# Kernel optimization log

Hardware: AMD Instinct MI355X
Metric: run time of the kernel (lower is better)

## Reference

```python
import jax, jax.numpy as jnp
import numpy as np

B, P, C = 256, 256, 512
EPS = 1e-6

def setup_inputs() -> dict:
    key = jax.random.key(0)
    ks = jax.random.split(key, 9)
    s_p = 1.0 / np.sqrt(P)
    s_c = 1.0 / np.sqrt(C)
    return {
        "x": jax.random.normal(ks[0], (B, P, C), dtype=jnp.float32),
        "ln_g": jnp.ones((C,), jnp.float32),
        "ln_b": jnp.zeros((C,), jnp.float32),
        # token-mixing MLP (P -> P -> P)
        "w1a": jax.random.normal(ks[1], (P, P), jnp.float32) * s_p,
        "b1a": jnp.zeros((P,), jnp.float32),
        "w1b": jax.random.normal(ks[2], (P, P), jnp.float32) * s_p,
        "b1b": jnp.zeros((P,), jnp.float32),
        # channel-mixing MLP (C -> C -> C)
        "w2a": jax.random.normal(ks[3], (C, C), jnp.float32) * s_c,
        "b2a": jnp.zeros((C,), jnp.float32),
        "w2b": jax.random.normal(ks[4], (C, C), jnp.float32) * s_c,
        "b2b": jnp.zeros((C,), jnp.float32),
    }

def _layernorm(v, g, b):
    mu = jnp.mean(v, axis=-1, keepdims=True)
    var = jnp.mean(jnp.square(v - mu), axis=-1, keepdims=True)
    return (v - mu) * jax.lax.rsqrt(var + EPS) * g + b

def reference(x, ln_g, ln_b, w1a, b1a, w1b, b1b, w2a, b2a, w2b, b2b):
    # token mixing: normalize, transpose to [B, C, P], MLP over P, transpose back
    h = _layernorm(x, ln_g, ln_b)                       # [B, P, C]
    ht = jnp.swapaxes(h, 1, 2)                          # [B, C, P]
    t = jax.nn.gelu(ht @ w1a + b1a, approximate=False) @ w1b + b1b
    x = jnp.swapaxes(t, 1, 2) + x                       # residual with original input
    # channel mixing: note residual adds to the NORMALIZED x (as in source)
    h = _layernorm(x, ln_g, ln_b)                       # [B, P, C]
    t2 = jax.nn.gelu(h @ w2a + b2a, approximate=False) @ w2b + b2b
    return h + t2
```

## Files before the change

### kernel.cpp

```cpp
#include <hip/hip_runtime.h>
#include <hip/hip_bf16.h>
#include <math.h>

typedef __bf16 bf16x8 __attribute__((ext_vector_type(8)));
typedef float f32x4 __attribute__((ext_vector_type(4)));
typedef unsigned short u16x8 __attribute__((ext_vector_type(8)));

#define DEV __device__ __forceinline__

DEV unsigned short f2bf(float f){ __hip_bfloat16 h=__float2bfloat16(f); unsigned short u; __builtin_memcpy(&u,&h,2); return u; }
DEV float bf2f(unsigned short u){ __hip_bfloat16 h; __builtin_memcpy(&h,&u,2); return __bfloat162float(h); }

DEV float gelu_f(float v){
  float u = v*(0.7978845608f + 0.0356774081f*v*v);
  float e = __expf(2.0f*u);
  float t = 1.0f - 2.0f*__builtin_amdgcn_rcpf(e + 1.0f);
  return 0.5f*v*(1.0f + t);
}

DEV void gl2lds16(const void* g, void* l){
  __builtin_amdgcn_global_load_lds((const __attribute__((address_space(1))) void*)g,
                                   (__attribute__((address_space(3))) void*)l, 16, 0, 0);
}

__global__ __launch_bounds__(256) void k_wt(const float* __restrict__ W,
                                            unsigned short* __restrict__ WT,
                                            int K, int N){
  int i = blockIdx.x*256 + threadIdx.x;
  if (i >= K*N) return;
  int k = i % K, n = i / K;
  WT[i] = f2bf(W[(size_t)k*N + n]);
}

__global__ __launch_bounds__(256) void k_ln1x(const float* __restrict__ x,
                                              const float* __restrict__ g,
                                              const float* __restrict__ be,
                                              unsigned short* __restrict__ ht,
                                              unsigned short* __restrict__ xb){
  __shared__ unsigned short tile[32][512];
  int blk = blockIdx.x;
  int b = blk >> 3, p0 = (blk & 7) << 5;
  int tid = threadIdx.x, w = tid >> 6, l = tid & 63;
  float4 gv0 = *(const float4*)(g  + l*8);
  float4 gv1 = *(const float4*)(g  + l*8 + 4);
  float4 bv0 = *(const float4*)(be + l*8);
  float4 bv1 = *(const float4*)(be + l*8 + 4);
  const float* xbase = x + (((size_t)b << 8) + p0) * 512;
  for (int i = 0; i < 8; ++i) {
    int pl = (i << 2) + w;
    const float* row = xbase + (size_t)pl*512 + l*8;
    float4 v0 = *(const float4*)row;
    float4 v1 = *(const float4*)(row + 4);
    u16x8 rc;
    rc[0]=f2bf(v0.x); rc[1]=f2bf(v0.y); rc[2]=f2bf(v0.z); rc[3]=f2bf(v0.w);
    rc[4]=f2bf(v1.x); rc[5]=f2bf(v1.y); rc[6]=f2bf(v1.z); rc[7]=f2bf(v1.w);
    *(u16x8*)(xb + (((size_t)b << 8) + p0 + pl)*512 + l*8) = rc;
    float s  = v0.x+v0.y+v0.z+v0.w + v1.x+v1.y+v1.z+v1.w;
    float s2 = v0.x*v0.x+v0.y*v0.y+v0.z*v0.z+v0.w*v0.w
             + v1.x*v1.x+v1.y*v1.y+v1.z*v1.z+v1.w*v1.w;
    #pragma unroll
    for (int off = 32; off; off >>= 1){ s += __shfl_xor(s, off); s2 += __shfl_xor(s2, off); }
    float mu = s * (1.0f/512.0f);
    float rs = rsqrtf(s2*(1.0f/512.0f) - mu*mu + 1e-6f);
    u16x8 o;
    o[0]=f2bf((v0.x-mu)*rs*gv0.x+bv0.x);
    o[1]=f2bf((v0.y-mu)*rs*gv0.y+bv0.y);
    o[2]=f2bf((v0.z-mu)*rs*gv0.z+bv0.z);
    o[3]=f2bf((v0.w-mu)*rs*gv0.w+bv0.w);
    o[4]=f2bf((v1.x-mu)*rs*gv1.x+bv1.x);
    o[5]=f2bf((v1.y-mu)*rs*gv1.y+bv1.y);
    o[6]=f2bf((v1.z-mu)*rs*gv1.z+bv1.z);
    o[7]=f2bf((v1.w-mu)*rs*gv1.w+bv1.w);
    *(u16x8*)(&tile[pl][l*8]) = o;
  }
  __syncthreads();
  unsigned short* hb = ht + ((size_t)b << 17);
  #pragma unroll
  for (int it = 0; it < 8; ++it) {
    int c = (it << 6) + (tid >> 2);
    int pch = (tid & 3) << 3;
    u16x8 o;
    #pragma unroll
    for (int j = 0; j < 8; ++j) o[j] = tile[pch + j][c];
    *(u16x8*)(hb + (size_t)c*256 + p0 + pch) = o;
  }
}

__global__ __launch_bounds__(256) void k_tl2(const unsigned short* __restrict__ t,
                                             const unsigned short* __restrict__ xb,
                                             const float* __restrict__ g,
                                             const float* __restrict__ be,
                                             unsigned short* __restrict__ h2){
  __shared__ unsigned short th[32][520];
  int blk = blockIdx.x;
  int b = blk >> 3, p0 = (blk & 7) << 5;
  int tid = threadIdx.x, w = tid >> 6, l = tid & 63;
  const unsigned short* tb = t + ((size_t)b << 17) + p0;
  #pragma unroll
  for (int it = 0; it < 8; ++it){
    int fc = (it << 8) + tid;
    int c = fc >> 2, pch = (fc & 3) << 3;
    u16x8 tv = *(const u16x8*)(tb + (size_t)c*256 + pch);
    #pragma unroll
    for (int j = 0; j < 8; ++j) th[pch + j][c] = tv[j];
  }
  __syncthreads();
  float4 gv0 = *(const float4*)(g  + l*8);
  float4 gv1 = *(const float4*)(g  + l*8 + 4);
  float4 bv0 = *(const float4*)(be + l*8);
  float4 bv1 = *(const float4*)(be + l*8 + 4);
  #pragma unroll
  for (int it = 0; it < 8; ++it){
    int pl = (it << 2) + w;
    u16x8 tvv = *(const u16x8*)(&th[pl][l*8]);
    size_t rowo = (((size_t)b << 8) + p0 + pl)*512 + l*8;
    u16x8 xvv = *(const u16x8*)(xb + rowo);
    float v[8];
    #pragma unroll
    for (int j = 0; j < 8; ++j) v[j] = bf2f(tvv[j]) + bf2f(xvv[j]);
    float s = 0.f, s2 = 0.f;
    #pragma unroll
    for (int j = 0; j < 8; ++j){ s += v[j]; s2 += v[j]*v[j]; }
    #pragma unroll
    for (int off = 32; off; off >>= 1){ s += __shfl_xor(s, off); s2 += __shfl_xor(s2, off); }
    float mu = s * (1.0f/512.0f);
    float rs = rsqrtf(s2*(1.0f/512.0f) - mu*mu + 1e-6f);
    u16x8 o;
    o[0]=f2bf((v[0]-mu)*rs*gv0.x+bv0.x);
    o[1]=f2bf((v[1]-mu)*rs*gv0.y+bv0.y);
    o[2]=f2bf((v[2]-mu)*rs*gv0.z+bv0.z);
    o[3]=f2bf((v[3]-mu)*rs*gv0.w+bv0.w);
    o[4]=f2bf((v[4]-mu)*rs*gv1.x+bv1.x);
    o[5]=f2bf((v[5]-mu)*rs*gv1.y+bv1.y);
    o[6]=f2bf((v[6]-mu)*rs*gv1.z+bv1.z);
    o[7]=f2bf((v[7]-mu)*rs*gv1.w+bv1.w);
    *(u16x8*)(h2 + rowo) = o;
  }
}

template<int N, int KT, int MODE>
__global__ __launch_bounds__(256, 2) void k_gemm(
    const unsigned short* __restrict__ A,
    const unsigned short* __restrict__ BT,
    const float* __restrict__ bias,
    unsigned short* __restrict__ outb,
    float* __restrict__ outf,
    const unsigned short* __restrict__ res)
{
  constexpr int K = KT*64;
  constexpr int nTn = N/128;
  constexpr int EPITCH = 176;
  constexpr int EREG   = 64*EPITCH;
  __shared__ char lds[4*EREG];
  char* lsA = lds;
  char* lsB = lds + 16384;

  int nwg = gridDim.x, bid = blockIdx.x;
  int wgid = ((nwg & 7) == 0) ? ((bid & 7)*(nwg >> 3) + (bid >> 3)) : bid;
  int tm = wgid / nTn, tn = wgid % nTn;
  size_t m0 = (size_t)tm * 128;
  int n0 = tn * 128;

  const int tid = threadIdx.x;
  const int w = tid >> 6, l = tid & 63;
  const int wm = w >> 1, wn = w & 1;
  const int la = l & 15, lg = l >> 4;

  f32x4 acc[4][4];
  #pragma unroll
  for (int i = 0; i < 4; ++i)
    #pragma unroll
    for (int j = 0; j < 4; ++j) acc[i][j] = (f32x4){0.f,0.f,0.f,0.f};

  for (int kt = 0; kt < KT; ++kt){
    int kb = kt << 6;
    #pragma unroll
    for (int i = 0; i < 4; ++i){
      int q = (i << 8) + tid;
      int row = q >> 3, sc = q & 7;
      int cc = sc ^ (row & 7);
      gl2lds16(A  + (m0 + row)*K + kb + (cc << 3), lsA + q*16);
      gl2lds16(BT + (size_t)(n0 + row)*K + kb + (cc << 3), lsB + q*16);
    }
    __syncthreads();
    #pragma unroll
    for (int ks = 0; ks < 2; ++ks){
      int c = (ks << 2) + lg;
      bf16x8 af[4], bfr[4];
      #pragma unroll
      for (int mi = 0; mi < 4; ++mi){
        int rr = (wm << 6) + (mi << 4) + la;
        af[mi] = *(const bf16x8*)(lsA + ((rr << 3) + (c ^ (rr & 7)))*16);
      }
      #pragma unroll
      for (int ni = 0; ni < 4; ++ni){
        int rn = (wn << 6) + (ni << 4) + la;
        bfr[ni] = *(const bf16x8*)(lsB + ((rn << 3) + (c ^ (rn & 7)))*16);
      }
      #pragma unroll
      for (int mi = 0; mi < 4; ++mi)
        #pragma unroll
        for (int ni = 0; ni < 4; ++ni)
          acc[mi][ni] = __builtin_amdgcn_mfma_f32_16x16x32_bf16(af[mi], bfr[ni], acc[mi][ni], 0, 0, 0);
    }
    __syncthreads();
  }

  char* ep = lds + w*EREG;
  #pragma unroll
  for (int ni = 0; ni < 4; ++ni){
    int colw = (ni << 4) + la;
    float bv = bias[n0 + (wn << 6) + colw];
    #pragma unroll
    for (int mi = 0; mi < 4; ++mi){
      #pragma unroll
      for (int rg = 0; rg < 4; ++rg){
        float v = acc[mi][ni][rg] + bv;
        if (MODE == 0) v = gelu_f(v);
        int r = (mi << 4) + (lg << 2) + rg;
        *(unsigned short*)(ep + r*EPITCH + colw*2) = f2bf(v);
      }
    }
  }
  __syncthreads();

  #pragma unroll
  for (int i = 0; i < 8; ++i){
    int q = (i << 8) + tid;
    int r = q >> 4, ck = q & 15;
    int wreg = ((r >> 6) << 1) | (ck >> 3);
    u16x8 val = *(const u16x8*)(lds + wreg*EREG + (r & 63)*EPITCH + (ck & 7)*16);
    size_t go = (m0 + r)*N + n0 + (ck << 3);
    if (MODE != 2){
      *(u16x8*)(outb + go) = val;
    } else {
      u16x8 rv = *(const u16x8*)(res + go);
      float4 o0, o1;
      o0.x = bf2f(val[0]) + bf2f(rv[0]);
      o0.y = bf2f(val[1]) + bf2f(rv[1]);
      o0.z = bf2f(val[2]) + bf2f(rv[2]);
      o0.w = bf2f(val[3]) + bf2f(rv[3]);
      o1.x = bf2f(val[4]) + bf2f(rv[4]);
      o1.y = bf2f(val[5]) + bf2f(rv[5]);
      o1.z = bf2f(val[6]) + bf2f(rv[6]);
      o1.w = bf2f(val[7]) + bf2f(rv[7]);
      *(float4*)(outf + go)     = o0;
      *(float4*)(outf + go + 4) = o1;
    }
  }
}

extern "C" void kernel_launch(void* const* d_in, const int* in_sizes, int n_in,
                              void* d_out, int out_size, void* d_ws, size_t ws_size,
                              hipStream_t stream) {
  const float* x   = (const float*)d_in[0];
  const float* lng = (const float*)d_in[1];
  const float* lnb = (const float*)d_in[2];
  const float* w1a = (const float*)d_in[3];
  const float* b1a = (const float*)d_in[4];
  const float* w1b = (const float*)d_in[5];
  const float* b1b = (const float*)d_in[6];
  const float* w2a = (const float*)d_in[7];
  const float* b2a = (const float*)d_in[8];
  const float* w2b = (const float*)d_in[9];
  const float* b2b = (const float*)d_in[10];
  float* out = (float*)d_out;
  char* ws = (char*)d_ws;
  unsigned short* bufA = (unsigned short*)ws;
  unsigned short* bufB = (unsigned short*)(ws + (size_t)(64u << 20));
  unsigned short* wt1a = (unsigned short*)(ws + (size_t)(128u << 20));
  unsigned short* wt1b = wt1a + 256*256;
  unsigned short* wt2a = wt1b + 256*256;
  unsigned short* wt2b = wt2a + 512*512;
  unsigned short* xb   = (unsigned short*)d_out;

  k_wt<<<256,  256, 0, stream>>>(w1a, wt1a, 256, 256);
  k_wt<<<256,  256, 0, stream>>>(w1b, wt1b, 256, 256);
  k_wt<<<1024, 256, 0, stream>>>(w2a, wt2a, 512, 512);
  k_wt<<<1024, 256, 0, stream>>>(w2b, wt2b, 512, 512);

  k_ln1x<<<2048, 256, 0, stream>>>(x, lng, lnb, bufA, xb);
  k_gemm<256, 4, 0><<<2048, 256, 0, stream>>>(bufA, wt1a, b1a, bufB, nullptr, nullptr);
  k_gemm<256, 4, 1><<<2048, 256, 0, stream>>>(bufB, wt1b, b1b, bufA, nullptr, nullptr);

  k_tl2<<<2048, 256, 0, stream>>>(bufA, xb, lng, lnb, bufB);

  k_gemm<512, 8, 0><<<2048, 256, 0, stream>>>(bufB, wt2a, b2a, bufA, nullptr, nullptr);
  k_gemm<512, 8, 2><<<2048, 256, 0, stream>>>(bufA, wt2b, b2b, nullptr, out, bufB);
}
```

Baseline: 293.2 us.

## Compute second token GEMM transposed to drop transpose in LN2 kernel

Replaces the second token-mixing GEMM with a transposed GEMM (W1b^T times activations) that writes its output directly in [B,P,C] layout. The LN2 kernel then becomes a simple row-wise, grid-strided pass with no LDS transpose. The change also merges the four weight-transpose launches into one kernel, and adds an XOR swizzle to the LN1 transpose tile to reduce LDS bank conflicts. The transposed GEMM reads the weights as the A operand and the activations as B, which may change the L2 reuse pattern.

```diff
diff --git a/kernel.cpp b/kernel.cpp
--- a/kernel.cpp
+++ b/kernel.cpp
@@ -23,13 +23,28 @@
                                    (__attribute__((address_space(3))) void*)l, 16, 0, 0);
 }
 
-__global__ __launch_bounds__(256) void k_wt(const float* __restrict__ W,
-                                            unsigned short* __restrict__ WT,
-                                            int K, int N){
+__global__ __launch_bounds__(256) void k_wt4(const float* __restrict__ w1a,
+                                             const float* __restrict__ w1b,
+                                             const float* __restrict__ w2a,
+                                             const float* __restrict__ w2b,
+                                             unsigned short* __restrict__ o1a,
+                                             unsigned short* __restrict__ o1b,
+                                             unsigned short* __restrict__ o2a,
+                                             unsigned short* __restrict__ o2b){
   int i = blockIdx.x*256 + threadIdx.x;
-  if (i >= K*N) return;
-  int k = i % K, n = i / K;
-  WT[i] = f2bf(W[(size_t)k*N + n]);
+  const float* W; unsigned short* O; int KN, j;
+  if (i < 131072){
+    if (i < 65536){ W = w1a; O = o1a; j = i; }
+    else          { W = w1b; O = o1b; j = i - 65536; }
+    KN = 256;
+  } else {
+    int i2 = i - 131072;
+    if (i2 < 262144){ W = w2a; O = o2a; j = i2; }
+    else            { W = w2b; O = o2b; j = i2 - 262144; }
+    KN = 512;
+  }
+  int k = j % KN, n = j / KN;
+  O[j] = f2bf(W[(size_t)k*KN + n]);
 }
 
 __global__ __launch_bounds__(256) void k_ln1x(const float* __restrict__ x,
@@ -46,6 +61,7 @@
   float4 bv0 = *(const float4*)(be + l*8);
   float4 bv1 = *(const float4*)(be + l*8 + 4);
   const float* xbase = x + (((size_t)b << 8) + p0) * 512;
+  #pragma unroll
   for (int i = 0; i < 8; ++i) {
     int pl = (i << 2) + w;
     const float* row = xbase + (size_t)pl*512 + l*8;
@@ -71,58 +87,45 @@
     o[5]=f2bf((v1.y-mu)*rs*gv1.y+bv1.y);
     o[6]=f2bf((v1.z-mu)*rs*gv1.z+bv1.z);
     o[7]=f2bf((v1.w-mu)*rs*gv1.w+bv1.w);
-    *(u16x8*)(&tile[pl][l*8]) = o;
+    *(u16x8*)(&tile[pl][(l ^ ((pl >> 3) << 1)) << 3]) = o;
   }
   __syncthreads();
   unsigned short* hb = ht + ((size_t)b << 17);
   #pragma unroll
   for (int it = 0; it < 8; ++it) {
     int c = (it << 6) + (tid >> 2);
-    int pch = (tid & 3) << 3;
+    int q = tid & 3, pch = q << 3;
+    int cs = c ^ (q << 4);
     u16x8 o;
     #pragma unroll
-    for (int j = 0; j < 8; ++j) o[j] = tile[pch + j][c];
+    for (int j = 0; j < 8; ++j) o[j] = tile[pch + j][cs];
     *(u16x8*)(hb + (size_t)c*256 + p0 + pch) = o;
   }
 }
 
-__global__ __launch_bounds__(256) void k_tl2(const unsigned short* __restrict__ t,
-                                             const unsigned short* __restrict__ xb,
-                                             const float* __restrict__ g,
-                                             const float* __restrict__ be,
-                                             unsigned short* __restrict__ h2){
-  __shared__ unsigned short th[32][520];
-  int blk = blockIdx.x;
-  int b = blk >> 3, p0 = (blk & 7) << 5;
+__global__ __launch_bounds__(256) void k_tl2s(const unsigned short* __restrict__ t,
+                                              const unsigned short* __restrict__ xb,
+                                              const float* __restrict__ g,
+                                              const float* __restrict__ be,
+                                              unsigned short* __restrict__ h2){
   int tid = threadIdx.x, w = tid >> 6, l = tid & 63;
-  const unsigned short* tb = t + ((size_t)b << 17) + p0;
-  #pragma unroll
-  for (int it = 0; it < 8; ++it){
-    int fc = (it << 8) + tid;
-    int c = fc >> 2, pch = (fc & 3) << 3;
-    u16x8 tv = *(const u16x8*)(tb + (size_t)c*256 + pch);
-    #pragma unroll
-    for (int j = 0; j < 8; ++j) th[pch + j][c] = tv[j];
-  }
-  __syncthreads();
   float4 gv0 = *(const float4*)(g  + l*8);
   float4 gv1 = *(const float4*)(g  + l*8 + 4);
   float4 bv0 = *(const float4*)(be + l*8);
   float4 bv1 = *(const float4*)(be + l*8 + 4);
-  #pragma unroll
-  for (int it = 0; it < 8; ++it){
-    int pl = (it << 2) + w;
-    u16x8 tvv = *(const u16x8*)(&th[pl][l*8]);
-    size_t rowo = (((size_t)b << 8) + p0 + pl)*512 + l*8;
-    u16x8 xvv = *(const u16x8*)(xb + rowo);
+  int wid = blockIdx.x*4 + w;
+  for (int r = wid; r < 65536; r += gridDim.x*4){
+    size_t off = (size_t)r*512 + l*8;
+    u16x8 tv = *(const u16x8*)(t + off);
+    u16x8 xv = *(const u16x8*)(xb + off);
     float v[8];
     #pragma unroll
-    for (int j = 0; j < 8; ++j) v[j] = bf2f(tvv[j]) + bf2f(xvv[j]);
+    for (int j = 0; j < 8; ++j) v[j] = bf2f(tv[j]) + bf2f(xv[j]);
     float s = 0.f, s2 = 0.f;
     #pragma unroll
     for (int j = 0; j < 8; ++j){ s += v[j]; s2 += v[j]*v[j]; }
     #pragma unroll
-    for (int off = 32; off; off >>= 1){ s += __shfl_xor(s, off); s2 += __shfl_xor(s2, off); }
+    for (int off2 = 32; off2; off2 >>= 1){ s += __shfl_xor(s, off2); s2 += __shfl_xor(s2, off2); }
     float mu = s * (1.0f/512.0f);
     float rs = rsqrtf(s2*(1.0f/512.0f) - mu*mu + 1e-6f);
     u16x8 o;
@@ -134,7 +137,7 @@
     o[5]=f2bf((v[5]-mu)*rs*gv1.y+bv1.y);
     o[6]=f2bf((v[6]-mu)*rs*gv1.z+bv1.z);
     o[7]=f2bf((v[7]-mu)*rs*gv1.w+bv1.w);
-    *(u16x8*)(h2 + rowo) = o;
+    *(u16x8*)(h2 + off) = o;
   }
 }
 
@@ -247,6 +250,99 @@
       *(float4*)(outf + go)     = o0;
       *(float4*)(outf + go + 4) = o1;
     }
+  }
+}
+
+__global__ __launch_bounds__(256, 2) void k_gemmT(
+    const unsigned short* __restrict__ A,
+    const unsigned short* __restrict__ BT,
+    const float* __restrict__ bias,
+    unsigned short* __restrict__ outb)
+{
+  constexpr int K = 256, KT = 4;
+  constexpr int EPITCH = 176;
+  constexpr int EREG   = 64*EPITCH;
+  __shared__ char lds[4*EREG];
+  char* lsA = lds;
+  char* lsB = lds + 16384;
+
+  int nwg = gridDim.x, bid = blockIdx.x;
+  int wgid = (bid & 7)*(nwg >> 3) + (bid >> 3);
+  int tm = wgid & 1, tn = wgid >> 1;
+  size_t m0 = (size_t)tm * 128;
+  int n0 = tn * 128;
+  int bb = n0 >> 9, c0 = n0 & 511;
+
+  const int tid = threadIdx.x;
+  const int w = tid >> 6, l = tid & 63;
+  const int wm = w >> 1, wn = w & 1;
+  const int la = l & 15, lg = l >> 4;
+
+  f32x4 acc[4][4];
+  #pragma unroll
+  for (int i = 0; i < 4; ++i)
+    #pragma unroll
+    for (int j = 0; j < 4; ++j) acc[i][j] = (f32x4){0.f,0.f,0.f,0.f};
+
+  for (int kt = 0; kt < KT; ++kt){
+    int kb = kt << 6;
+    #pragma unroll
+    for (int i = 0; i < 4; ++i){
+      int q = (i << 8) + tid;
+      int row = q >> 3, sc = q & 7;
+      int cc = sc ^ (row & 7);
+      gl2lds16(A  + (m0 + row)*K + kb + (cc << 3), lsA + q*16);
+      gl2lds16(BT + (size_t)(n0 + row)*K + kb + (cc << 3), lsB + q*16);
+    }
+    __syncthreads();
+    #pragma unroll
+    for (int ks = 0; ks < 2; ++ks){
+      int c = (ks << 2) + lg;
+      bf16x8 af[4], bfr[4];
+      #pragma unroll
+      for (int mi = 0; mi < 4; ++mi){
+        int rr = (wm << 6) + (mi << 4) + la;
+        af[mi] = *(const bf16x8*)(lsA + ((rr << 3) + (c ^ (rr & 7)))*16);
+      }
+      #pragma unroll
+      for (int ni = 0; ni < 4; ++ni){
+        int rn = (wn << 6) + (ni << 4) + la;
+        bfr[ni] = *(const bf16x8*)(lsB + ((rn << 3) + (c ^ (rn & 7)))*16);
+      }
+      #pragma unroll
+      for (int mi = 0; mi < 4; ++mi)
+        #pragma unroll
+        for (int ni = 0; ni < 4; ++ni)
+          acc[mi][ni] = __builtin_amdgcn_mfma_f32_16x16x32_bf16(af[mi], bfr[ni], acc[mi][ni], 0, 0, 0);
+    }
+    __syncthreads();
+  }
+
+  char* ep = lds + w*EREG;
+  #pragma unroll
+  for (int mi = 0; mi < 4; ++mi){
+    int rb = (mi << 4) + (lg << 2);
+    float4 bq = *(const float4*)(bias + m0 + (wm << 6) + rb);
+    #pragma unroll
+    for (int ni = 0; ni < 4; ++ni){
+      int colw = (ni << 4) + la;
+      #pragma unroll
+      for (int rg = 0; rg < 4; ++rg){
+        float v = acc[mi][ni][rg] + ((const float*)&bq)[rg];
+        *(unsigned short*)(ep + (rb + rg)*EPITCH + colw*2) = f2bf(v);
+      }
+    }
+  }
+  __syncthreads();
+
+  #pragma unroll
+  for (int i = 0; i < 8; ++i){
+    int q = (i << 8) + tid;
+    int r = q >> 4, ck = q & 15;
+    int wreg = ((r >> 6) << 1) | (ck >> 3);
+    u16x8 val = *(const u16x8*)(lds + wreg*EREG + (r & 63)*EPITCH + (ck & 7)*16);
+    size_t go = ((size_t)bb << 17) + (m0 + r)*512 + c0 + (ck << 3);
+    *(u16x8*)(outb + go) = val;
   }
 }
 
@@ -274,16 +370,13 @@
   unsigned short* wt2b = wt2a + 512*512;
   unsigned short* xb   = (unsigned short*)d_out;
 
-  k_wt<<<256,  256, 0, stream>>>(w1a, wt1a, 256, 256);
-  k_wt<<<256,  256, 0, stream>>>(w1b, wt1b, 256, 256);
-  k_wt<<<1024, 256, 0, stream>>>(w2a, wt2a, 512, 512);
-  k_wt<<<1024, 256, 0, stream>>>(w2b, wt2b, 512, 512);
+  k_wt4<<<2560, 256, 0, stream>>>(w1a, w1b, w2a, w2b, wt1a, wt1b, wt2a, wt2b);
 
   k_ln1x<<<2048, 256, 0, stream>>>(x, lng, lnb, bufA, xb);
   k_gemm<256, 4, 0><<<2048, 256, 0, stream>>>(bufA, wt1a, b1a, bufB, nullptr, nullptr);
-  k_gemm<256, 4, 1><<<2048, 256, 0, stream>>>(bufB, wt1b, b1b, bufA, nullptr, nullptr);
-
-  k_tl2<<<2048, 256, 0, stream>>>(bufA, xb, lng, lnb, bufB);
+  k_gemmT<<<2048, 256, 0, stream>>>(wt1b, bufB, b1b, bufA);
+
+  k_tl2s<<<2048, 256, 0, stream>>>(bufA, xb, lng, lnb, bufB);
 
   k_gemm<512, 8, 0><<<2048, 256, 0, stream>>>(bufB, wt2a, b2a, bufA, nullptr, nullptr);
   k_gemm<512, 8, 2><<<2048, 256, 0, stream>>>(bufA, wt2b, b2b, nullptr, out, bufB);
```

Measured after the change: 280.7 us. -4.3%, faster.
